# Kernel tuning notes

Measured on AMD Instinct MI355X. Metric: run time of the kernel, lower is better.

## Reference

```python
import jax, jax.numpy as jnp
import numpy as np

B, T, C = 2, 2048, 1024
H, HS = 16, 64          # num_heads, head_size; H*HS == C
FF = 4 * C
EPS = 1e-5


def setup_inputs() -> dict:
    key = jax.random.key(0)
    ks = jax.random.split(key, 10)
    s = 0.02
    return {
        "x": jax.random.normal(ks[0], (B, T, C), dtype=jnp.float32),
        "Wq": jax.random.normal(ks[1], (H, C, HS), dtype=jnp.float32) * s,
        "Wk": jax.random.normal(ks[2], (H, C, HS), dtype=jnp.float32) * s,
        "Wv": jax.random.normal(ks[3], (H, C, HS), dtype=jnp.float32) * s,
        "p": jnp.ones((H,), dtype=jnp.float32),  # per-head learnable scale, init 1
        "Wproj": jax.random.normal(ks[4], (C, C), dtype=jnp.float32) * s,
        "W1": jax.random.normal(ks[5], (C, FF), dtype=jnp.float32) * s,
        "W2": jax.random.normal(ks[6], (FF, C), dtype=jnp.float32) * s,
        "ln1_w": jnp.ones((C,), dtype=jnp.float32),
        "ln1_b": jnp.zeros((C,), dtype=jnp.float32),
        "ln2_w": jnp.ones((C,), dtype=jnp.float32),
        "ln2_b": jnp.zeros((C,), dtype=jnp.float32),
    }


def _layernorm(x, w, b):
    mu = jnp.mean(x, axis=-1, keepdims=True)
    var = jnp.mean(jnp.square(x - mu), axis=-1, keepdims=True)
    return (x - mu) * jax.lax.rsqrt(var + EPS) * w + b


def reference(x, Wq, Wk, Wv, p, Wproj, W1, W2, ln1_w, ln1_b, ln2_w, ln2_b):
    # --- multi-head causal self-attention (dropout p=0 -> identity) ---
    h = _layernorm(x, ln1_w, ln1_b)
    q = jnp.einsum("btc,hcs->bhts", h, Wq)  # [B,H,T,HS]
    k = jnp.einsum("btc,hcs->bhts", h, Wk)
    v = jnp.einsum("btc,hcs->bhts", h, Wv)
    scale = p ** (-0.5)  # per-head scale, p init to 1
    wei = jnp.einsum("bhts,bhks->bhtk", q, k) * scale[None, :, None, None]
    causal = jnp.tril(jnp.ones((T, T), dtype=bool))
    wei = jnp.where(causal[None, None], wei, -jnp.inf)
    wei = jax.nn.softmax(wei, axis=-1)
    att = jnp.einsum("bhtk,bhks->bhts", wei, v)          # [B,H,T,HS]
    att = att.transpose(0, 2, 1, 3).reshape(B, T, C)     # concat heads
    sa = att @ Wproj
    x = x + sa
    # --- feed-forward (activation_id=0 -> ReLU) ---
    h2 = _layernorm(x, ln2_w, ln2_b)
    ff = jax.nn.relu(h2 @ W1) @ W2
    return x + ff
```

## Files before the change

### kernel.cpp

```cpp
#include <hip/hip_runtime.h>


typedef _Float16 f16;
typedef _Float16 f16x8 __attribute__((ext_vector_type(8)));
typedef _Float16 f16x4v __attribute__((ext_vector_type(4)));
typedef float f32x4 __attribute__((ext_vector_type(4)));

static constexpr int Tn = 2048;
static constexpr int Cn = 1024;
static constexpr int HSn = 64;

__device__ __forceinline__ void glds16(const f16* g, f16* l) {
    __builtin_amdgcn_global_load_lds((const __attribute__((address_space(1))) void*)g,
                                     (__attribute__((address_space(3))) void*)l,
                                     16, 0, 0);
}

__global__ __launch_bounds__(256) void ln_kernel(const float* __restrict__ x,
                                                 const float* __restrict__ w,
                                                 const float* __restrict__ b,
                                                 f16* __restrict__ out) {
    int row = blockIdx.x;
    const float* xr = x + (size_t)row * Cn;
    int tid = threadIdx.x, l = tid & 63, wv = tid >> 6;
    float4 v = *(const float4*)(xr + tid * 4);
    float s = v.x + v.y + v.z + v.w;
    float sq = v.x * v.x + v.y * v.y + v.z * v.z + v.w * v.w;
#pragma unroll
    for (int off = 32; off > 0; off >>= 1) {
        s += __shfl_down(s, off);
        sq += __shfl_down(sq, off);
    }
    __shared__ float red[8];
    if (l == 0) { red[wv] = s; red[wv + 4] = sq; }
    __syncthreads();
    float ts = red[0] + red[1] + red[2] + red[3];
    float tq = red[4] + red[5] + red[6] + red[7];
    float mean = ts * (1.0f / Cn);
    float var = tq * (1.0f / Cn) - mean * mean;
    float rstd = rsqrtf(var + 1e-5f);
    float4 wv4 = *(const float4*)(w + tid * 4);
    float4 bv4 = *(const float4*)(b + tid * 4);
    f16x4v o;
    o[0] = (f16)((v.x - mean) * rstd * wv4.x + bv4.x);
    o[1] = (f16)((v.y - mean) * rstd * wv4.y + bv4.y);
    o[2] = (f16)((v.z - mean) * rstd * wv4.z + bv4.z);
    o[3] = (f16)((v.w - mean) * rstd * wv4.w + bv4.w);
    *(f16x4v*)(out + (size_t)row * Cn + tid * 4) = o;
}

__global__ __launch_bounds__(256) void tr_cast_f32(const float* __restrict__ in, int irs,
                                                   f16* __restrict__ out, int ors) {
    __shared__ float tile[32][33];
    int r0 = blockIdx.x * 32, c0 = blockIdx.y * 32;
    int t = threadIdx.x;
    int rr = t >> 3, c4 = (t & 7) * 4;
    float4 v = *(const float4*)(in + (size_t)(r0 + rr) * irs + c0 + c4);
    tile[rr][c4] = v.x; tile[rr][c4 + 1] = v.y; tile[rr][c4 + 2] = v.z; tile[rr][c4 + 3] = v.w;
    __syncthreads();
    int cc = t >> 3, r4 = (t & 7) * 4;
    f16x4v o;
    o[0] = (f16)tile[r4][cc];
    o[1] = (f16)tile[r4 + 1][cc];
    o[2] = (f16)tile[r4 + 2][cc];
    o[3] = (f16)tile[r4 + 3][cc];
    *(f16x4v*)(out + (size_t)(c0 + cc) * ors + r0 + r4) = o;
}

__global__ __launch_bounds__(256) void tr_cast_qkv(const float* __restrict__ Wq,
                                                   const float* __restrict__ Wk,
                                                   const float* __restrict__ Wv,
                                                   f16* __restrict__ out) {
    int z = blockIdx.z;
    int qkv = z >> 4, h = z & 15;
    const float* in = (qkv == 0 ? Wq : qkv == 1 ? Wk : Wv) + (size_t)h * Cn * HSn;
    f16* o = out + (size_t)(qkv * Cn + h * HSn) * Cn;
    __shared__ float tile[32][33];
    int r0 = blockIdx.x * 32, c0 = blockIdx.y * 32;
    int t = threadIdx.x;
    int rr = t >> 3, c4 = (t & 7) * 4;
    float4 v = *(const float4*)(in + (size_t)(r0 + rr) * HSn + c0 + c4);
    tile[rr][c4] = v.x; tile[rr][c4 + 1] = v.y; tile[rr][c4 + 2] = v.z; tile[rr][c4 + 3] = v.w;
    __syncthreads();
    int cc = t >> 3, r4 = (t & 7) * 4;
    f16x4v ov;
    ov[0] = (f16)tile[r4][cc];
    ov[1] = (f16)tile[r4 + 1][cc];
    ov[2] = (f16)tile[r4 + 2][cc];
    ov[3] = (f16)tile[r4 + 3][cc];
    *(f16x4v*)(o + (size_t)(c0 + cc) * Cn + r0 + r4) = ov;
}

__global__ __launch_bounds__(256) void tr_vT(const f16* __restrict__ QKV, f16* __restrict__ vT) {
    int bh = blockIdx.z;
    int b = bh >> 4, h = bh & 15;
    const f16* in = QKV + (size_t)b * Tn * 3072 + 2048 + h * HSn;
    f16* out = vT + (size_t)bh * HSn * Tn;
    int r0 = blockIdx.x * 64;
    __shared__ __align__(16) f16 tile[64][72];
    int t = threadIdx.x;
#pragma unroll
    for (int i = 0; i < 2; i++) {
        int f = i * 256 + t;
        int rr = f >> 3, c8 = (f & 7) * 8;
        *(uint4*)(&tile[rr][c8]) = *(const uint4*)(in + (size_t)(r0 + rr) * 3072 + c8);
    }
    __syncthreads();
#pragma unroll
    for (int i = 0; i < 2; i++) {
        int f = i * 256 + t;
        int cc = f >> 3, r8 = (f & 7) * 8;
        union { f16 h[8]; uint4 v; } u;
#pragma unroll
        for (int j = 0; j < 8; j++) u.h[j] = tile[r8 + j][cc];
        *(uint4*)(out + (size_t)cc * Tn + r0 + r8) = u.v;
    }
}

__device__ __forceinline__ void l2_map(int& bm, int& bn) {
    int wg = blockIdx.y * 32 + blockIdx.x;
    int x = wg & 7, idx = wg >> 3;
    bm = x * 4 + (idx & 3);
    bn = idx >> 2;
}

template <int EPI>
__global__ __launch_bounds__(256) void gemm_bt(const f16* __restrict__ A, const f16* __restrict__ Bt,
                                               void* __restrict__ Cout, const float* __restrict__ resid,
                                               int M, int N, int K) {
    __shared__ __align__(16) f16 As[2][4096];
    __shared__ __align__(16) f16 Bs[2][4096];
    int bm, bn;
    l2_map(bm, bn);
    int tid = threadIdx.x, l = tid & 63, w = tid >> 6;
    int wr = w >> 1, wc = w & 1;
    f32x4 acc[4][4];
#pragma unroll
    for (int m = 0; m < 4; m++)
#pragma unroll
        for (int n = 0; n < 4; n++) acc[m][n] = f32x4{0.f, 0.f, 0.f, 0.f};

    const f16* ag = A + (size_t)(bm * 128 + (tid >> 2)) * K + (tid & 3) * 8;
    const f16* bg = Bt + (size_t)(bn * 128 + (tid >> 2)) * K + (tid & 3) * 8;
    const size_t half = (size_t)64 * K;
    int KT = K >> 5;
    int rbase = (wr * 64 + (l & 15)) * 32 + (l >> 4) * 8;
    int cbase = (wc * 64 + (l & 15)) * 32 + (l >> 4) * 8;

    auto stage = [&](int kt, int bf) {
        int k0 = kt * 32;
        glds16(ag + k0, &As[bf][w * 512]);
        glds16(ag + half + k0, &As[bf][2048 + w * 512]);
        glds16(bg + k0, &Bs[bf][w * 512]);
        glds16(bg + half + k0, &Bs[bf][2048 + w * 512]);
    };

    stage(0, 0);
    __syncthreads();
    for (int kt = 0; kt < KT; ++kt) {
        int cb = kt & 1;
        if (kt + 1 < KT) stage(kt + 1, cb ^ 1);
        f16x8 af[4], bfr[4];
#pragma unroll
        for (int m = 0; m < 4; m++) af[m] = *(const f16x8*)(&As[cb][rbase + m * 512]);
#pragma unroll
        for (int n = 0; n < 4; n++) bfr[n] = *(const f16x8*)(&Bs[cb][cbase + n * 512]);
#pragma unroll
        for (int m = 0; m < 4; m++)
#pragma unroll
            for (int n = 0; n < 4; n++)
                acc[m][n] = __builtin_amdgcn_mfma_f32_16x16x32_f16(af[m], bfr[n], acc[m][n], 0, 0, 0);
        __syncthreads();
    }

    int row0 = bm * 128 + wr * 64 + (l >> 4) * 4;
    int col0 = bn * 128 + wc * 64 + (l & 15);
#pragma unroll
    for (int m = 0; m < 4; m++) {
#pragma unroll
        for (int n = 0; n < 4; n++) {
#pragma unroll
            for (int r = 0; r < 4; r++) {
                size_t idx = (size_t)(row0 + m * 16 + r) * N + (col0 + n * 16);
                float v = acc[m][n][r];
                if constexpr (EPI == 0) ((f16*)Cout)[idx] = (f16)v;
                else if constexpr (EPI == 1) ((f16*)Cout)[idx] = (f16)fmaxf(v, 0.f);
                else ((float*)Cout)[idx] = v + resid[idx];
            }
        }
    }
}

template <int EPI>
__global__ __launch_bounds__(512) void gemm_ks(const f16* __restrict__ A, const f16* __restrict__ Bt,
                                               void* __restrict__ Cout, const float* __restrict__ resid,
                                               int M, int N, int K) {
    __shared__ __align__(16) char smem[65536];
    f16* As = (f16*)smem;
    f16* Bs = (f16*)(smem + 32768);
    int bm, bn;
    l2_map(bm, bn);
    int tid = threadIdx.x, l = tid & 63, w = tid >> 6;
    int grp = w >> 2, wl = w & 3;
    int wr = wl >> 1, wc = wl & 1;
    int Kh = K >> 1;
    int KT = Kh >> 5;

    f32x4 acc[4][4];
#pragma unroll
    for (int m = 0; m < 4; m++)
#pragma unroll
        for (int n = 0; n < 4; n++) acc[m][n] = f32x4{0.f, 0.f, 0.f, 0.f};

    const f16* agp = A + (size_t)(bm * 128 + wl * 16 + (l >> 2)) * K + grp * Kh + (l & 3) * 8;
    const f16* bgp = Bt + (size_t)(bn * 128 + wl * 16 + (l >> 2)) * K + grp * Kh + (l & 3) * 8;
    const size_t half = (size_t)64 * K;
    f16* Ab = As + grp * 8192;
    f16* Bb = Bs + grp * 8192;

    auto stage = [&](int kt, int bf) {
        size_t k0 = (size_t)kt * 32;
        glds16(agp + k0, Ab + bf * 4096 + wl * 512);
        glds16(agp + half + k0, Ab + bf * 4096 + 2048 + wl * 512);
        glds16(bgp + k0, Bb + bf * 4096 + wl * 512);
        glds16(bgp + half + k0, Bb + bf * 4096 + 2048 + wl * 512);
    };

    int rbase = (wr * 64 + (l & 15)) * 32 + (l >> 4) * 8;
    int cbase = (wc * 64 + (l & 15)) * 32 + (l >> 4) * 8;

    stage(0, 0);
    __syncthreads();
    for (int kt = 0; kt < KT; ++kt) {
        int cb = kt & 1;
        if (kt + 1 < KT) stage(kt + 1, cb ^ 1);
        f16x8 af[4], bfr[4];
#pragma unroll
        for (int m = 0; m < 4; m++) af[m] = *(const f16x8*)(Ab + cb * 4096 + rbase + m * 512);
#pragma unroll
        for (int n = 0; n < 4; n++) bfr[n] = *(const f16x8*)(Bb + cb * 4096 + cbase + n * 512);
#pragma unroll
        for (int m = 0; m < 4; m++)
#pragma unroll
            for (int n = 0; n < 4; n++)
                acc[m][n] = __builtin_amdgcn_mfma_f32_16x16x32_f16(af[m], bfr[n], acc[m][n], 0, 0, 0);
        __syncthreads();
    }

    float* red = (float*)smem;
#pragma unroll
    for (int m = 0; m < 4; m++) {
        if (grp == 1) {
#pragma unroll
            for (int n = 0; n < 4; n++)
                *(f32x4*)(red + wl * 1280 + l * 20 + n * 4) = acc[m][n];
        }
        __syncthreads();
        if (grp == 0) {
#pragma unroll
            for (int n = 0; n < 4; n++)
                acc[m][n] += *(const f32x4*)(red + wl * 1280 + l * 20 + n * 4);
        }
        __syncthreads();
    }

    if (grp == 0) {
        int row0 = bm * 128 + wr * 64 + (l >> 4) * 4;
        int col0 = bn * 128 + wc * 64 + (l & 15);
#pragma unroll
        for (int m = 0; m < 4; m++) {
#pragma unroll
            for (int n = 0; n < 4; n++) {
#pragma unroll
                for (int r = 0; r < 4; r++) {
                    size_t idx = (size_t)(row0 + m * 16 + r) * N + (col0 + n * 16);
                    float v = acc[m][n][r];
                    if constexpr (EPI == 0) ((f16*)Cout)[idx] = (f16)v;
                    else if constexpr (EPI == 1) ((f16*)Cout)[idx] = (f16)fmaxf(v, 0.f);
                    else ((float*)Cout)[idx] = v + resid[idx];
                }
            }
        }
    }
}

__global__ __launch_bounds__(256) void attn_kernel(const f16* __restrict__ QKV,
                                                   const f16* __restrict__ vT,
                                                   const float* __restrict__ p,
                                                   f16* __restrict__ att) {
    int wg = blockIdx.x;
    int x = wg & 7, idx = wg >> 3;
    int bh = x * 4 + (idx & 3);
    int pq = idx >> 2;
    int b = bh >> 4, h = bh & 15;
    int tid = threadIdx.x, w = tid >> 6, l = tid & 63;
    float sc2 = rsqrtf(p[h]) * 1.44269504f;

    __shared__ __align__(16) f16 Ks[2][4096];
    __shared__ __align__(16) f16 Vs[2][4096];
    __shared__ __align__(16) f16 Ps[4][16 * 80];
    f16* Pw = &Ps[w][0];

    int srow0 = tid >> 3;
    int c0 = (tid & 7) ^ (srow0 & 7);
    int srow1 = 32 + srow0;
    int c1 = (tid & 7) ^ (srow1 & 7);
    const f16* Kg = QKV + (size_t)b * Tn * 3072 + 1024 + h * HSn;
    const f16* Vg = vT + (size_t)bh * HSn * Tn;

    auto stageKV = [&](int kv0, int bf) {
        glds16(Kg + (size_t)(kv0 + srow0) * 3072 + c0 * 8, &Ks[bf][w * 512]);
        glds16(Kg + (size_t)(kv0 + srow1) * 3072 + c1 * 8, &Ks[bf][2048 + w * 512]);
        glds16(Vg + (size_t)srow0 * Tn + kv0 + c0 * 8, &Vs[bf][w * 512]);
        glds16(Vg + (size_t)srow1 * Tn + kv0 + c1 * 8, &Vs[bf][2048 + w * 512]);
    };

    for (int pass = 0; pass < 2; ++pass) {
        int qt = pass ? (31 - pq) : pq;
        int qg = qt * 64 + w * 16 + (l & 15);
        int qo = qt * 64 + w * 16 + (l >> 4) * 4;
        const f16* qptr = QKV + (size_t)(b * Tn + qg) * 3072 + h * HSn + (l >> 4) * 8;
        f16x8 qf0 = *(const f16x8*)(qptr);
        f16x8 qf1 = *(const f16x8*)(qptr + 32);
        f16 sch = (f16)sc2;
#pragma unroll
        for (int j = 0; j < 8; j++) { qf0[j] *= sch; qf1[j] *= sch; }

        f32x4 o[4];
#pragma unroll
        for (int nf = 0; nf < 4; nf++) o[nf] = f32x4{0.f, 0.f, 0.f, 0.f};
        float m_r = -1e30f, l_r = 0.f;

        int nt = qt + 1;
        stageKV(0, 0);
        __syncthreads();
        for (int t = 0; t < nt; ++t) {
            int cb = t & 1, kv0 = t * 64;
            if (t + 1 < nt) stageKV(kv0 + 64, cb ^ 1);
            const char* Kb = (const char*)&Ks[cb][0];
            const char* Vb = (const char*)&Vs[cb][0];
            f32x4 s[4];
#pragma unroll
            for (int n = 0; n < 4; n++) s[n] = f32x4{0.f, 0.f, 0.f, 0.f};
            __builtin_amdgcn_s_setprio(1);
#pragma unroll
            for (int n = 0; n < 4; n++) {
#pragma unroll
                for (int ks = 0; ks < 2; ks++) {
                    int boff = (n * 16 + (l & 15)) * 128 + (((ks * 32 + (l >> 4) * 8) * 2) ^ ((l & 7) << 4));
                    f16x8 kf = *(const f16x8*)(Kb + boff);
                    s[n] = __builtin_amdgcn_mfma_f32_16x16x32_f16(kf, ks == 0 ? qf0 : qf1, s[n], 0, 0, 0);
                }
            }
            __builtin_amdgcn_s_setprio(0);
            if (t == qt) {
                int rel = qg - kv0;
#pragma unroll
                for (int n = 0; n < 4; n++)
#pragma unroll
                    for (int r = 0; r < 4; r++) {
                        int kvr = n * 16 + (l >> 4) * 4 + r;
                        if (kvr > rel) s[n][r] = -1e30f;
                    }
            }
            float tmax = -1e30f;
#pragma unroll
            for (int n = 0; n < 4; n++)
#pragma unroll
                for (int r = 0; r < 4; r++) tmax = fmaxf(tmax, s[n][r]);
            tmax = fmaxf(tmax, __shfl_xor(tmax, 16));
            tmax = fmaxf(tmax, __shfl_xor(tmax, 32));
            float lmul = 1.f;
            if (__any(tmax > m_r + 8.f)) {
                float mnew = fmaxf(m_r, tmax);
                lmul = exp2f(m_r - mnew);
                m_r = mnew;
                float ar[4];
#pragma unroll
                for (int r = 0; r < 4; r++) ar[r] = __shfl(lmul, (l >> 4) * 4 + r);
#pragma unroll
                for (int nf = 0; nf < 4; nf++)
#pragma unroll
                    for (int r = 0; r < 4; r++) o[nf][r] *= ar[r];
            }
            float rsum = 0.f;
#pragma unroll
            for (int n = 0; n < 4; n++) {
                f16x4v pk;
#pragma unroll
                for (int r = 0; r < 4; r++) {
                    float e = exp2f(s[n][r] - m_r);
                    rsum += e;
                    pk[r] = (f16)e;
                }
                *(f16x4v*)(&Pw[(l & 15) * 80 + n * 16 + (l >> 4) * 4]) = pk;
            }
            rsum += __shfl_xor(rsum, 16);
            rsum += __shfl_xor(rsum, 32);
            l_r = l_r * lmul + rsum;
            f16x8 pa0 = *(const f16x8*)(&Pw[(l & 15) * 80 + (l >> 4) * 8]);
            f16x8 pa1 = *(const f16x8*)(&Pw[(l & 15) * 80 + 32 + (l >> 4) * 8]);
            __builtin_amdgcn_s_setprio(1);
#pragma unroll
            for (int nf = 0; nf < 4; nf++) {
#pragma unroll
                for (int ks = 0; ks < 2; ks++) {
                    int boff = (nf * 16 + (l & 15)) * 128 + (((ks * 32 + (l >> 4) * 8) * 2) ^ ((l & 7) << 4));
                    f16x8 vf = *(const f16x8*)(Vb + boff);
                    o[nf] = __builtin_amdgcn_mfma_f32_16x16x32_f16(ks == 0 ? pa0 : pa1, vf, o[nf], 0, 0, 0);
                }
            }
            __builtin_amdgcn_s_setprio(0);
            __syncthreads();
        }
        float lro[4];
#pragma unroll
        for (int r = 0; r < 4; r++) lro[r] = __shfl(l_r, (l >> 4) * 4 + r);
#pragma unroll
        for (int nf = 0; nf < 4; nf++) {
#pragma unroll
            for (int r = 0; r < 4; r++) {
                float v = o[nf][r] / lro[r];
                att[(size_t)(b * Tn + qo + r) * Cn + h * HSn + nf * 16 + (l & 15)] = (f16)v;
            }
        }
    }
}

extern "C" void kernel_launch(void* const* d_in, const int* in_sizes, int n_in,
                              void* d_out, int out_size, void* d_ws, size_t ws_size,
                              hipStream_t stream) {
    const float* x = (const float*)d_in[0];
    const float* Wq = (const float*)d_in[1];
    const float* Wk = (const float*)d_in[2];
    const float* Wv = (const float*)d_in[3];
    const float* p = (const float*)d_in[4];
    const float* Wproj = (const float*)d_in[5];
    const float* W1 = (const float*)d_in[6];
    const float* W2 = (const float*)d_in[7];
    const float* ln1w = (const float*)d_in[8];
    const float* ln1b = (const float*)d_in[9];
    const float* ln2w = (const float*)d_in[10];
    const float* ln2b = (const float*)d_in[11];

    char* ws = (char*)d_ws;
    const size_t MB = 1ull << 20;
    f16* Wqkv_t = (f16*)(ws + 0 * MB);
    f16* Wproj_t = (f16*)(ws + 6 * MB);
    f16* W1_t = (f16*)(ws + 8 * MB);
    f16* W2_t = (f16*)(ws + 16 * MB);
    float* x1 = (float*)(ws + 24 * MB);
    f16* QKV = (f16*)(ws + 40 * MB);
    f16* h1 = (f16*)(ws + 64 * MB);
    f16* vTb = (f16*)(ws + 64 * MB);
    f16* attb = (f16*)(ws + 72 * MB);
    f16* h2 = attb;
    f16* ffh = QKV;
    float* out = (float*)d_out;

    tr_cast_qkv<<<dim3(32, 2, 48), 256, 0, stream>>>(Wq, Wk, Wv, Wqkv_t);
    tr_cast_f32<<<dim3(32, 32), 256, 0, stream>>>(Wproj, 1024, Wproj_t, 1024);
    tr_cast_f32<<<dim3(32, 128), 256, 0, stream>>>(W1, 4096, W1_t, 1024);
    tr_cast_f32<<<dim3(128, 32), 256, 0, stream>>>(W2, 1024, W2_t, 4096);

    ln_kernel<<<4096, 256, 0, stream>>>(x, ln1w, ln1b, h1);
    gemm_bt<0><<<dim3(32, 24), 256, 0, stream>>>(h1, Wqkv_t, QKV, nullptr, 4096, 3072, 1024);
    tr_vT<<<dim3(32, 1, 32), 256, 0, stream>>>(QKV, vTb);
    attn_kernel<<<512, 256, 0, stream>>>(QKV, vTb, p, attb);
    gemm_ks<2><<<dim3(32, 8), 512, 0, stream>>>(attb, Wproj_t, x1, x, 4096, 1024, 1024);
    ln_kernel<<<4096, 256, 0, stream>>>(x1, ln2w, ln2b, h2);
    gemm_bt<1><<<dim3(32, 32), 256, 0, stream>>>(h2, W1_t, ffh, nullptr, 4096, 4096, 1024);
    gemm_ks<2><<<dim3(32, 8), 512, 0, stream>>>(ffh, W2_t, out, x1, 4096, 1024, 4096);
}
```

Before: 253.3 us.

## Replace QKV and FFN1 GEMMs with 256x256-tile, 4-stage pipelined 8-wave kernel

Adds gemm8, a 512-thread GEMM with 256x256 output tiles, a four-buffer LDS pipeline of async global-to-LDS loads using explicit vmcnt waits and raw barriers, XOR-swizzled LDS layout to avoid bank conflicts, and setprio around MFMA bursts. It replaces the 128x128 double-buffered gemm_bt for the QKV projection and the first FFN layer. The aim is more data reuse per tile and better hiding of load latency. In exchange it launches far fewer workgroups (192/256), which may leave CUs underfilled, and it relies on hand-tuned wait counts being correct.

```diff
diff --git a/kernel.cpp b/kernel.cpp
--- a/kernel.cpp
+++ b/kernel.cpp
@@ -14,6 +14,13 @@
     __builtin_amdgcn_global_load_lds((const __attribute__((address_space(1))) void*)g,
                                      (__attribute__((address_space(3))) void*)l,
                                      16, 0, 0);
+}
+
+#define VMCNT(N) asm volatile("s_waitcnt vmcnt(" #N ")" ::: "memory")
+__device__ __forceinline__ void barrier_raw() {
+    asm volatile("" ::: "memory");
+    __builtin_amdgcn_s_barrier();
+    asm volatile("" ::: "memory");
 }
 
 __global__ __launch_bounds__(256) void ln_kernel(const float* __restrict__ x,
@@ -117,78 +124,102 @@
     }
 }
 
+template <int EPI>
+__global__ __launch_bounds__(512, 2) void gemm8(const f16* __restrict__ A, const f16* __restrict__ Bt,
+                                                f16* __restrict__ Cout, int M, int N, int K) {
+    __shared__ __align__(16) f16 Abuf[4][8192];
+    __shared__ __align__(16) f16 Bbuf[4][8192];
+    int wg = blockIdx.x;
+    int xcd = wg & 7, idx = wg >> 3;
+    int bm = xcd * 2 + (idx & 1), bn = idx >> 1;
+    int tid = threadIdx.x, l = tid & 63, w = tid >> 6;
+    int wr = w >> 2, wc = w & 3;
+
+    f32x4 acc[8][4];
+#pragma unroll
+    for (int m = 0; m < 8; m++)
+#pragma unroll
+        for (int n = 0; n < 4; n++) acc[m][n] = f32x4{0.f, 0.f, 0.f, 0.f};
+
+    int l15 = l & 15;
+    int lane_off = l15 * 32 + (((l >> 4) ^ ((l15 >> 1) & 3)) << 3);
+    const f16* Afr = &Abuf[0][wr * 4096 + lane_off];
+    const f16* Bfr = &Bbuf[0][(wc >> 1) * 4096 + (wc & 1) * 2048 + lane_off];
+
+    int srow = w * 16 + (l >> 2);
+    int schunk = (l & 3) ^ ((l >> 3) & 3);
+    const f16* agp = A + (size_t)(bm * 256 + srow) * K + schunk * 8;
+    const f16* bgp = Bt + (size_t)(bn * 256 + srow) * K + schunk * 8;
+    const size_t rK = (size_t)128 * K;
+    f16* dstA = &Abuf[0][w * 512];
+    f16* dstB = &Bbuf[0][w * 512];
+
+    auto stage = [&](int kt, int bf) {
+        int k0 = kt * 32;
+        glds16(agp + k0, dstA + bf * 8192);
+        glds16(agp + rK + k0, dstA + bf * 8192 + 4096);
+        glds16(bgp + k0, dstB + bf * 8192);
+        glds16(bgp + rK + k0, dstB + bf * 8192 + 4096);
+    };
+
+    int NT = K >> 5;
+    stage(0, 0);
+    stage(1, 1);
+    stage(2, 2);
+    for (int t = 0; t < NT; ++t) {
+        int cb = t & 3;
+        VMCNT(8);
+        barrier_raw();
+        const f16* Ab = Afr + cb * 8192;
+        const f16* Bb = Bfr + cb * 8192;
+        f16x8 af[4], bf4[4];
+#pragma unroll
+        for (int m = 0; m < 4; m++) af[m] = *(const f16x8*)(Ab + m * 512);
+#pragma unroll
+        for (int n = 0; n < 4; n++) bf4[n] = *(const f16x8*)(Bb + n * 512);
+        if (t + 3 < NT) stage(t + 3, (t + 3) & 3);
+        __builtin_amdgcn_s_setprio(1);
+#pragma unroll
+        for (int m = 0; m < 4; m++)
+#pragma unroll
+            for (int n = 0; n < 4; n++)
+                acc[m][n] = __builtin_amdgcn_mfma_f32_16x16x32_f16(af[m], bf4[n], acc[m][n], 0, 0, 0);
+        __builtin_amdgcn_s_setprio(0);
+        barrier_raw();
+#pragma unroll
+        for (int m = 0; m < 4; m++) af[m] = *(const f16x8*)(Ab + (m + 4) * 512);
+        __builtin_amdgcn_s_setprio(1);
+#pragma unroll
+        for (int m = 0; m < 4; m++)
+#pragma unroll
+            for (int n = 0; n < 4; n++)
+                acc[m + 4][n] = __builtin_amdgcn_mfma_f32_16x16x32_f16(af[m], bf4[n], acc[m + 4][n], 0, 0, 0);
+        __builtin_amdgcn_s_setprio(0);
+    }
+    VMCNT(0);
+
+    int row0 = bm * 256 + wr * 128 + (l >> 4) * 4;
+    int col0 = bn * 256 + wc * 64 + (l & 15);
+#pragma unroll
+    for (int m = 0; m < 8; m++) {
+#pragma unroll
+        for (int n = 0; n < 4; n++) {
+#pragma unroll
+            for (int r = 0; r < 4; r++) {
+                size_t idx = (size_t)(row0 + m * 16 + r) * N + (col0 + n * 16);
+                float v = acc[m][n][r];
+                if constexpr (EPI == 1) v = fmaxf(v, 0.f);
+                Cout[idx] = (f16)v;
+            }
+        }
+    }
+}
+
 __device__ __forceinline__ void l2_map(int& bm, int& bn) {
     int wg = blockIdx.y * 32 + blockIdx.x;
     int x = wg & 7, idx = wg >> 3;
     bm = x * 4 + (idx & 3);
     bn = idx >> 2;
-}
-
-template <int EPI>
-__global__ __launch_bounds__(256) void gemm_bt(const f16* __restrict__ A, const f16* __restrict__ Bt,
-                                               void* __restrict__ Cout, const float* __restrict__ resid,
-                                               int M, int N, int K) {
-    __shared__ __align__(16) f16 As[2][4096];
-    __shared__ __align__(16) f16 Bs[2][4096];
-    int bm, bn;
-    l2_map(bm, bn);
-    int tid = threadIdx.x, l = tid & 63, w = tid >> 6;
-    int wr = w >> 1, wc = w & 1;
-    f32x4 acc[4][4];
-#pragma unroll
-    for (int m = 0; m < 4; m++)
-#pragma unroll
-        for (int n = 0; n < 4; n++) acc[m][n] = f32x4{0.f, 0.f, 0.f, 0.f};
-
-    const f16* ag = A + (size_t)(bm * 128 + (tid >> 2)) * K + (tid & 3) * 8;
-    const f16* bg = Bt + (size_t)(bn * 128 + (tid >> 2)) * K + (tid & 3) * 8;
-    const size_t half = (size_t)64 * K;
-    int KT = K >> 5;
-    int rbase = (wr * 64 + (l & 15)) * 32 + (l >> 4) * 8;
-    int cbase = (wc * 64 + (l & 15)) * 32 + (l >> 4) * 8;
-
-    auto stage = [&](int kt, int bf) {
-        int k0 = kt * 32;
-        glds16(ag + k0, &As[bf][w * 512]);
-        glds16(ag + half + k0, &As[bf][2048 + w * 512]);
-        glds16(bg + k0, &Bs[bf][w * 512]);
-        glds16(bg + half + k0, &Bs[bf][2048 + w * 512]);
-    };
-
-    stage(0, 0);
-    __syncthreads();
-    for (int kt = 0; kt < KT; ++kt) {
-        int cb = kt & 1;
-        if (kt + 1 < KT) stage(kt + 1, cb ^ 1);
-        f16x8 af[4], bfr[4];
-#pragma unroll
-        for (int m = 0; m < 4; m++) af[m] = *(const f16x8*)(&As[cb][rbase + m * 512]);
-#pragma unroll
-        for (int n = 0; n < 4; n++) bfr[n] = *(const f16x8*)(&Bs[cb][cbase + n * 512]);
-#pragma unroll
-        for (int m = 0; m < 4; m++)
-#pragma unroll
-            for (int n = 0; n < 4; n++)
-                acc[m][n] = __builtin_amdgcn_mfma_f32_16x16x32_f16(af[m], bfr[n], acc[m][n], 0, 0, 0);
-        __syncthreads();
-    }
-
-    int row0 = bm * 128 + wr * 64 + (l >> 4) * 4;
-    int col0 = bn * 128 + wc * 64 + (l & 15);
-#pragma unroll
-    for (int m = 0; m < 4; m++) {
-#pragma unroll
-        for (int n = 0; n < 4; n++) {
-#pragma unroll
-            for (int r = 0; r < 4; r++) {
-                size_t idx = (size_t)(row0 + m * 16 + r) * N + (col0 + n * 16);
-                float v = acc[m][n][r];
-                if constexpr (EPI == 0) ((f16*)Cout)[idx] = (f16)v;
-                else if constexpr (EPI == 1) ((f16*)Cout)[idx] = (f16)fmaxf(v, 0.f);
-                else ((float*)Cout)[idx] = v + resid[idx];
-            }
-        }
-    }
 }
 
 template <int EPI>
@@ -464,11 +495,11 @@
     tr_cast_f32<<<dim3(128, 32), 256, 0, stream>>>(W2, 1024, W2_t, 4096);
 
     ln_kernel<<<4096, 256, 0, stream>>>(x, ln1w, ln1b, h1);
-    gemm_bt<0><<<dim3(32, 24), 256, 0, stream>>>(h1, Wqkv_t, QKV, nullptr, 4096, 3072, 1024);
+    gemm8<0><<<192, 512, 0, stream>>>(h1, Wqkv_t, QKV, 4096, 3072, 1024);
     tr_vT<<<dim3(32, 1, 32), 256, 0, stream>>>(QKV, vTb);
     attn_kernel<<<512, 256, 0, stream>>>(QKV, vTb, p, attb);
     gemm_ks<2><<<dim3(32, 8), 512, 0, stream>>>(attb, Wproj_t, x1, x, 4096, 1024, 1024);
     ln_kernel<<<4096, 256, 0, stream>>>(x1, ln2w, ln2b, h2);
-    gemm_bt<1><<<dim3(32, 32), 256, 0, stream>>>(h2, W1_t, ffh, nullptr, 4096, 4096, 1024);
+    gemm8<1><<<256, 512, 0, stream>>>(h2, W1_t, ffh, 4096, 4096, 1024);
     gemm_ks<2><<<dim3(32, 8), 512, 0, stream>>>(ffh, W2_t, out, x1, 4096, 1024, 4096);
 }
```

After: 243.1 us. 4.0% less time.
